# Optimization experiments

Hardware: AMD Instinct MI355X
Metric: run time of the kernel (lower is better)

Reference implementation:

```python
import jax, jax.numpy as jnp
import numpy as np
from jax import lax

IMG_SIZE = 640
STRIDES = (8, 16, 32)
NA = 3          # anchors per level
NC = 80         # classes
CONF_THRESH = 0.001
NMS_THRESH = 0.6
ANCHORS = np.array([[10,13],[16,30],[33,23],[30,61],[62,45],[59,119],[116,90],[156,198],[373,326]], np.float32).reshape(3, 3, 2)

def _make_grids():
    gs, st, aw = [], [], []
    for i, s in enumerate(STRIDES):
        hs = ws = IMG_SIZE // s
        gy, gx = np.meshgrid(np.arange(hs), np.arange(ws), indexing='ij')
        gxy = np.stack([gx, gy], -1).astype(np.float32).reshape(1, hs*ws, 1, 2)
        gs.append(gxy)
        st.append(np.full((1, hs*ws, NA, 2), s, np.float32))
        aw.append(np.tile(ANCHORS[i][None], (hs*ws, 1, 1)))
    return (np.concatenate(gs, 1), np.concatenate(st, 1), np.concatenate(aw, 0)[None])

GRID_CELL, STRIDE_T, ANCH_WH = _make_grids()  # [1,HW,1,2], [1,HW,3,2], [1,HW,3,2]

def _nms_classaware(boxes, score, valid):
    # Greedy NMS, class-aware via coordinate offset already applied to boxes.
    # Faithful to the numpy baseline: w,h = max(1e-28, .), areas without +1.
    x1, y1, x2, y2 = boxes[:, 0], boxes[:, 1], boxes[:, 2], boxes[:, 3]
    areas = (x2 - x1) * (y2 - y1)
    order = jnp.argsort(-score)
    N = boxes.shape[0]
    def body(i, state):
        supp, keep = state
        idx = order[i]
        active = jnp.logical_and(jnp.logical_not(supp[idx]), valid[idx])
        keep = keep.at[idx].set(active)
        xx1 = jnp.maximum(x1[idx], x1)
        yy1 = jnp.maximum(y1[idx], y1)
        xx2 = jnp.minimum(x2[idx], x2)
        yy2 = jnp.minimum(y2[idx], y2)
        w = jnp.maximum(1e-28, xx2 - xx1)
        h = jnp.maximum(1e-28, yy2 - yy1)
        inter = w * h
        iou = inter / (areas[idx] + areas - inter)
        newsupp = jnp.logical_and(iou > NMS_THRESH, active)
        newsupp = newsupp.at[idx].set(False)
        return jnp.logical_or(supp, newsupp), keep
    supp0 = jnp.zeros((N,), bool)
    keep0 = jnp.zeros((N,), bool)
    _, keep = lax.fori_loop(0, N, body, (supp0, keep0))
    return keep

def _decode_and_nms(pred_s, pred_m, pred_l):
    objs, clss, regs = [], [], []
    for pred in (pred_s, pred_m, pred_l):
        B, C, H, W = pred.shape
        p = pred.transpose(0, 2, 3, 1).reshape(B, H*W, C)
        objs.append(p[..., :NA].reshape(B, H*W*NA, 1))
        clss.append(p[..., NA:NA*(1+NC)].reshape(B, H*W*NA, NC))
        regs.append(p[..., NA*(1+NC):].reshape(B, H*W, NA, 4))
    obj_pred = jnp.concatenate(objs, axis=1)   # [B, N, 1]
    cls_pred = jnp.concatenate(clss, axis=1)   # [B, N, NC]
    reg_pred = jnp.concatenate(regs, axis=1)   # [B, HW, 3, 4]
    grid = jnp.asarray(GRID_CELL)
    stride = jnp.asarray(STRIDE_T)
    anch = jnp.asarray(ANCH_WH)
    B = reg_pred.shape[0]
    c_xy = (jax.nn.sigmoid(reg_pred[..., :2]) + grid) * stride
    b_wh = jnp.exp(reg_pred[..., 2:]) * anch
    xywh = jnp.concatenate([c_xy, b_wh], -1).reshape(B, -1, 4)
    x1y1 = xywh[..., :2] - xywh[..., 2:] / 2
    x2y2 = xywh[..., :2] + xywh[..., 2:] / 2
    boxes = jnp.clip(jnp.concatenate([x1y1, x2y2], -1) / IMG_SIZE, 0.0, 1.0)[0]  # [N,4]
    obj_s = jax.nn.sigmoid(obj_pred)[0]                     # [N,1]
    scores_all = jax.nn.softmax(cls_pred[0], axis=1) * obj_s  # [N,NC]
    cls_ind = jnp.argmax(scores_all, axis=1)                # [N]
    score = jnp.max(scores_all, axis=1)                     # [N]
    valid = score >= CONF_THRESH
    # class-aware NMS: offset normalized boxes by 2*class so classes never overlap
    boxes_off = boxes + cls_ind[:, None].astype(boxes.dtype) * 2.0
    keep = _nms_classaware(lax.stop_gradient(boxes_off), lax.stop_gradient(score), valid)
    out = jnp.concatenate([
        boxes,                                    # 4 cols
        score[:, None],                           # 1 col
        cls_ind[:, None].astype(boxes.dtype),     # 1 col (non-diff)
        keep[:, None].astype(boxes.dtype),        # 1 col (non-diff)
    ], axis=1)                                    # [N, 7]
    return out

def setup_inputs() -> dict:
    key = jax.random.key(0)
    k1, k2, k3 = jax.random.split(key, 3)
    return {
        'pred_s': jax.random.normal(k1, (1, 255, 80, 80), jnp.float32),
        'pred_m': jax.random.normal(k2, (1, 255, 40, 40), jnp.float32),
        'pred_l': jax.random.normal(k3, (1, 255, 20, 20), jnp.float32),
    }

def reference(pred_s, pred_m, pred_l):
    return _decode_and_nms(pred_s, pred_m, pred_l)
```

## Files before the change

kernel.cpp:

```cpp
#include <hip/hip_runtime.h>
#include <cstdint>

#define NPRED 25200
#define NPOS  8400
#define NCLS  80
#define CAP   512
#define CSTRIDE 16
#define MW    8
#define NCHUNK 132

__device__ __forceinline__ float sigmoidf_(float x) { return 1.0f / (1.0f + expf(-x)); }

__global__ __launch_bounds__(64) void decode_kernel(
    const float* __restrict__ ps, const float* __restrict__ pm, const float* __restrict__ pl,
    float* __restrict__ out, int* __restrict__ counts,
    float4* __restrict__ g_boxin, uint64_t* __restrict__ g_key)
{
    int chunk = blockIdx.x;
    int a     = blockIdx.y;
    int t     = threadIdx.x;

    const float* p; int HW, W, base, si; float stride; int w0;
    if (chunk < 100)      { p = ps; HW = 6400; W = 80; stride = 8.f;  base = 0;    si = 0; w0 = chunk * 64; }
    else if (chunk < 125) { p = pm; HW = 1600; W = 40; stride = 16.f; base = 6400; si = 1; w0 = (chunk - 100) * 64; }
    else                  { p = pl; HW = 400;  W = 20; stride = 32.f; base = 8000; si = 2; w0 = (chunk - 125) * 64; }

    int local = w0 + t;
    bool valid = local < HW;
    int lclamp = valid ? local : (HW - 1);

    __shared__ float lds[NCLS * 64];

    const float* cbase = p + (size_t)(3 + a * NCLS) * HW;
    int lane_c = t >> 4;
    int j      = (t & 15) << 2;
    int off    = w0 + j; if (off > HW - 4) off = HW - 4;

    float4 vreg[20];
#pragma unroll
    for (int r0 = 0; r0 < 20; r0++)
        vreg[r0] = *(const float4*)(cbase + (size_t)(r0 * 4 + lane_c) * HW + off);
    float objl = p[(size_t)a * HW + lclamp];
    const float* rb = p + (size_t)(3 + 3 * NCLS + a * 4) * HW + lclamp;
    float tx = rb[0], ty = rb[(size_t)HW], tw = rb[(size_t)2 * HW], th = rb[(size_t)3 * HW];
#pragma unroll
    for (int r0 = 0; r0 < 20; r0++)
        *(float4*)&lds[(r0 * 4 + lane_c) * 64 + j] = vreg[r0];
    __syncthreads();

    float m = -INFINITY;
#pragma unroll 16
    for (int c = 0; c < NCLS; c++) m = fmaxf(m, lds[c * 64 + t]);
    float s = 0.f;
#pragma unroll 16
    for (int c = 0; c < NCLS; c++) {
        float e = expf(lds[c * 64 + t] - m);
        lds[c * 64 + t] = e;
        s += e;
    }
    float obj = sigmoidf_(objl);
    float best = -1.f; int bi = 0;
#pragma unroll 16
    for (int c = 0; c < NCLS; c++) {
        float sc = lds[c * 64 + t] / s * obj;
        if (sc > best) { best = sc; bi = c; }
    }

    if (!valid) return;

    const float AW[9] = {10.f,16.f,33.f, 30.f,62.f,59.f, 116.f,156.f,373.f};
    const float AH[9] = {13.f,30.f,23.f, 61.f,45.f,119.f, 90.f,198.f,326.f};
    float aw = AW[si*3 + a], ah = AH[si*3 + a];

    int y = local / W;
    int x = local - y * W;
    float cx = (sigmoidf_(tx) + (float)x) * stride;
    float cy = (sigmoidf_(ty) + (float)y) * stride;
    float bw = expf(tw) * aw;
    float bh = expf(th) * ah;
    float x1 = fminf(fmaxf((cx - bw / 2.f) / 640.f, 0.f), 1.f);
    float y1 = fminf(fmaxf((cy - bh / 2.f) / 640.f, 0.f), 1.f);
    float x2 = fminf(fmaxf((cx + bw / 2.f) / 640.f, 0.f), 1.f);
    float y2 = fminf(fmaxf((cy + bh / 2.f) / 640.f, 0.f), 1.f);

    int g = (base + local) * 3 + a;
    float clsf = (float)bi;
    float* o = out + (size_t)g * 7;
    o[0] = x1; o[1] = y1; o[2] = x2; o[3] = y2;
    o[4] = best; o[5] = clsf; o[6] = 0.f;

    if (best >= 0.001f) {
        int slot = atomicAdd(&counts[bi * CSTRIDE], 1);
        if (slot < CAP) {
            float off2 = clsf * 2.0f;
            g_boxin[bi * CAP + slot] = make_float4(x1 + off2, y1 + off2,
                                                   x2 + off2, y2 + off2);
            unsigned u = __float_as_uint(best);
            u = (u & 0x80000000u) ? ~u : (u | 0x80000000u);
            g_key[bi * CAP + slot] = ((uint64_t)(~u) << 15) | (uint64_t)g;
        }
    }
}

__global__ __launch_bounds__(256) void nms_sort_kernel(
    const int* __restrict__ counts, const uint64_t* __restrict__ g_key,
    const float4* __restrict__ g_boxin, float4* __restrict__ g_sbox,
    int* __restrict__ g_sg)
{
    int c  = blockIdx.x;
    int i0 = blockIdx.y << 6;
    int n = counts[c * CSTRIDE]; if (n > CAP) n = CAP;
    if (i0 >= n) return;
    int tid = threadIdx.x;

    __shared__ uint64_t key[CAP];
    for (int i = tid; i < n; i += 256) key[i] = g_key[c * CAP + i];
    __syncthreads();

    int item = i0 + (tid >> 2);
    int sub  = tid & 3;
    bool act = item < n;
    int r = 0;
    uint64_t k = 0;
    if (act) {
        k = key[item];
        int nq = (n + 3) >> 2;
        int lo = sub * nq; if (lo > n) lo = n;
        int hi = lo + nq;  if (hi > n) hi = n;
        int jj = lo;
        for (; jj + 8 <= hi; jj += 8) {
            int t0 = key[jj]   < k, t1 = key[jj+1] < k;
            int t2 = key[jj+2] < k, t3 = key[jj+3] < k;
            int t4 = key[jj+4] < k, t5 = key[jj+5] < k;
            int t6 = key[jj+6] < k, t7 = key[jj+7] < k;
            r += t0 + t1 + t2 + t3 + t4 + t5 + t6 + t7;
        }
        for (; jj < hi; jj++) r += (key[jj] < k);
    }
    r += __shfl_xor(r, 1);
    r += __shfl_xor(r, 2);
    if (act && sub == 0) {
        g_sbox[c * CAP + r] = g_boxin[c * CAP + item];
        g_sg[c * CAP + r] = (int)(k & 0x7FFF);
    }
}

__global__ __launch_bounds__(256) void nms_build_kernel(
    const int* __restrict__ counts, const float4* __restrict__ g_sbox,
    uint64_t* __restrict__ g_mask)
{
    int c = blockIdx.x;
    int w = blockIdx.y;
    int n = counts[c * CSTRIDE]; if (n > CAP) n = CAP;
    int j0 = w << 6;
    if (j0 >= n) return;
    int j1 = j0 + 64; if (j1 > n) j1 = n;
    int cnt = j1 - j0;
    int tid = threadIdx.x;

    __shared__ float4 sb[64];
    if (tid < 64) {
        float4 sv = make_float4(3e30f, 3e30f, 3e30f, 3e30f);
        if (tid < cnt) sv = g_sbox[c * CAP + j0 + tid];
        sb[tid] = sv;
    }
    __syncthreads();

    uint64_t* gm = g_mask + (size_t)c * MW * CAP + (size_t)w * CAP;
    for (int i = tid; i < n; i += 256) {
        float4 b4 = g_sbox[c * CAP + i];
        float Ai = (b4.z - b4.x) * (b4.w - b4.y);
        uint64_t bits = 0;
        if (i + 1 < j1) {
#pragma unroll 8
            for (int jq = 0; jq < 64; jq++) {
                float4 bj = sb[jq];
                float xx1 = fmaxf(b4.x, bj.x);
                float yy1 = fmaxf(b4.y, bj.y);
                float xx2 = fminf(b4.z, bj.z);
                float yy2 = fminf(b4.w, bj.w);
                float ww = fmaxf(1e-28f, xx2 - xx1);
                float hh = fmaxf(1e-28f, yy2 - yy1);
                float inter = ww * hh;
                float Aj = (bj.z - bj.x) * (bj.w - bj.y);
                float iou = inter / ((Ai + Aj) - inter);
                if ((j0 + jq) > i && iou > 0.6f) bits |= 1ull << jq;
            }
        }
        gm[i] = bits;
    }
}

__global__ __launch_bounds__(64) void nms_scan_kernel(
    const int* __restrict__ counts, const int* __restrict__ g_sg,
    const uint64_t* __restrict__ g_mask, float* __restrict__ out)
{
    int c = blockIdx.x;
    int n = counts[c * CSTRIDE]; if (n > CAP) n = CAP;
    int nw = (n + 63) >> 6;
    int lane = threadIdx.x;

    const uint64_t* gm = g_mask + (size_t)c * MW * CAP;
    const int* sg = g_sg + c * CAP;

    uint64_t removed = 0;
    for (int w = 0; w < nw; w++) {
        uint64_t rw = __shfl(removed, w);
        int row = (w << 6) + lane;
        uint64_t diag = (row < n) ? gm[w * CAP + row] : 0ull;
        int rem = n - (w << 6);
        uint64_t valid = (rem >= 64) ? ~0ull : ((1ull << rem) - 1ull);
        uint64_t nulls = __ballot(diag == 0ull);
        uint64_t cand = ~rw & valid;
        uint64_t kw = 0;
        uint64_t it = cand & ~nulls;
        while (it) {
            int b = __ffsll((unsigned long long)it) - 1;
            kw |= 1ull << b;
            uint64_t db = __shfl(diag, b);
            it &= ~db; cand &= ~db;
            it &= ~(1ull << b);
        }
        kw |= cand & nulls;

        int g  = lane >> 3;
        int wp = lane & 7;
        uint64_t acc = 0;
        if (wp < nw) {
            uint64_t mybits = kw & (0xFFull << (g * 8));
            while (mybits) {
                int b = __ffsll((unsigned long long)mybits) - 1;
                mybits &= mybits - 1;
                acc |= gm[wp * CAP + ((w << 6) + b)];
            }
        }
        acc |= __shfl_xor(acc, 8);
        acc |= __shfl_xor(acc, 16);
        acc |= __shfl_xor(acc, 32);
        if (lane < MW) removed |= acc;

        if (row < n && ((kw >> lane) & 1))
            out[(size_t)sg[row] * 7 + 6] = 1.0f;
    }
}

extern "C" void kernel_launch(void* const* d_in, const int* in_sizes, int n_in,
                              void* d_out, int out_size, void* d_ws, size_t ws_size,
                              hipStream_t stream) {
    const float* ps = (const float*)d_in[0];
    const float* pm = (const float*)d_in[1];
    const float* pl = (const float*)d_in[2];
    float* out = (float*)d_out;

    char* ws = (char*)d_ws;
    int*      counts  = (int*)ws;
    float4*   g_boxin = (float4*)(ws + 8192);
    uint64_t* g_key   = (uint64_t*)(ws + 663552);
    float4*   g_sbox  = (float4*)(ws + 991232);
    int*      g_sg    = (int*)(ws + 1646592);
    uint64_t* g_mask  = (uint64_t*)(ws + 1810432);

    hipMemsetAsync(counts, 0, 8192, stream);
    decode_kernel<<<dim3(NCHUNK, 3), 64, 0, stream>>>(ps, pm, pl, out, counts, g_boxin, g_key);
    nms_sort_kernel<<<dim3(NCLS, MW), 256, 0, stream>>>(counts, g_key, g_boxin, g_sbox, g_sg);
    nms_build_kernel<<<dim3(NCLS, MW), 256, 0, stream>>>(counts, g_sbox, g_mask);
    nms_scan_kernel<<<NCLS, 64, 0, stream>>>(counts, g_sg, g_mask, out);
}
```

Measured before the change: 111.4 us.

## Fuse NMS sort, mask build and scan into one per-class kernel

Replaces the three NMS kernels (sort, mask build, scan) with a single kernel that runs one 256-thread block per class. Sorted boxes, indices and the IoU mask now live in shared memory instead of global workspace. This removes two kernel launches and the global round trips between stages. In exchange each class gets one block of 256 threads instead of up to eight blocks per stage, so less of the GPU works in parallel, and the block's shared-memory footprint grows to roughly 46 KB.

```diff
diff --git a/kernel.cpp b/kernel.cpp
--- a/kernel.cpp
+++ b/kernel.cpp
@@ -102,145 +102,113 @@
     }
 }
 
-__global__ __launch_bounds__(256) void nms_sort_kernel(
-    const int* __restrict__ counts, const uint64_t* __restrict__ g_key,
-    const float4* __restrict__ g_boxin, float4* __restrict__ g_sbox,
-    int* __restrict__ g_sg)
+__global__ __launch_bounds__(256) void nms_fused_kernel(
+    const int* __restrict__ counts, const float4* __restrict__ g_boxin,
+    const uint64_t* __restrict__ g_key, float* __restrict__ out)
 {
-    int c  = blockIdx.x;
-    int i0 = blockIdx.y << 6;
+    int c = blockIdx.x;
     int n = counts[c * CSTRIDE]; if (n > CAP) n = CAP;
-    if (i0 >= n) return;
+    if (n == 0) return;
+    int nw = (n + 63) >> 6;
     int tid = threadIdx.x;
 
     __shared__ uint64_t key[CAP];
+    __shared__ float4   sbox[CAP];
+    __shared__ int      sg[CAP];
+    __shared__ uint64_t mask[MW * CAP];
+    __shared__ uint64_t keptw[MW];
+
     for (int i = tid; i < n; i += 256) key[i] = g_key[c * CAP + i];
-    __syncthreads();
-
-    int item = i0 + (tid >> 2);
-    int sub  = tid & 3;
-    bool act = item < n;
-    int r = 0;
-    uint64_t k = 0;
-    if (act) {
-        k = key[item];
-        int nq = (n + 3) >> 2;
-        int lo = sub * nq; if (lo > n) lo = n;
-        int hi = lo + nq;  if (hi > n) hi = n;
-        int jj = lo;
-        for (; jj + 8 <= hi; jj += 8) {
+    for (int i = n + tid; i < nw * 64; i += 256)
+        sbox[i] = make_float4(3e30f, 3e30f, 3e30f, 3e30f);
+    __syncthreads();
+
+    for (int i = tid; i < n; i += 256) {
+        uint64_t k = key[i];
+        int r = 0, jj = 0;
+        for (; jj + 8 <= n; jj += 8) {
             int t0 = key[jj]   < k, t1 = key[jj+1] < k;
             int t2 = key[jj+2] < k, t3 = key[jj+3] < k;
             int t4 = key[jj+4] < k, t5 = key[jj+5] < k;
             int t6 = key[jj+6] < k, t7 = key[jj+7] < k;
             r += t0 + t1 + t2 + t3 + t4 + t5 + t6 + t7;
         }
-        for (; jj < hi; jj++) r += (key[jj] < k);
-    }
-    r += __shfl_xor(r, 1);
-    r += __shfl_xor(r, 2);
-    if (act && sub == 0) {
-        g_sbox[c * CAP + r] = g_boxin[c * CAP + item];
-        g_sg[c * CAP + r] = (int)(k & 0x7FFF);
-    }
-}
-
-__global__ __launch_bounds__(256) void nms_build_kernel(
-    const int* __restrict__ counts, const float4* __restrict__ g_sbox,
-    uint64_t* __restrict__ g_mask)
-{
-    int c = blockIdx.x;
-    int w = blockIdx.y;
-    int n = counts[c * CSTRIDE]; if (n > CAP) n = CAP;
-    int j0 = w << 6;
-    if (j0 >= n) return;
-    int j1 = j0 + 64; if (j1 > n) j1 = n;
-    int cnt = j1 - j0;
-    int tid = threadIdx.x;
-
-    __shared__ float4 sb[64];
+        for (; jj < n; jj++) r += (key[jj] < k);
+        sbox[r] = g_boxin[c * CAP + i];
+        sg[r] = (int)(k & 0x7FFF);
+    }
+    __syncthreads();
+
+    for (int w = 0; w < nw; w++) {
+        int j0 = w << 6;
+        int j1 = j0 + 64; if (j1 > n) j1 = n;
+        for (int i = tid; i < n; i += 256) {
+            float4 b4 = sbox[i];
+            float Ai = (b4.z - b4.x) * (b4.w - b4.y);
+            uint64_t bits = 0;
+            if (i + 1 < j1) {
+#pragma unroll 8
+                for (int jq = 0; jq < 64; jq++) {
+                    float4 bj = sbox[j0 + jq];
+                    float xx1 = fmaxf(b4.x, bj.x);
+                    float yy1 = fmaxf(b4.y, bj.y);
+                    float xx2 = fminf(b4.z, bj.z);
+                    float yy2 = fminf(b4.w, bj.w);
+                    float ww = fmaxf(1e-28f, xx2 - xx1);
+                    float hh = fmaxf(1e-28f, yy2 - yy1);
+                    float inter = ww * hh;
+                    float Aj = (bj.z - bj.x) * (bj.w - bj.y);
+                    float iou = inter / ((Ai + Aj) - inter);
+                    if ((j0 + jq) > i && (j0 + jq) < j1 && iou > 0.6f)
+                        bits |= 1ull << jq;
+                }
+            }
+            mask[w * CAP + i] = bits;
+        }
+    }
+    __syncthreads();
+
     if (tid < 64) {
-        float4 sv = make_float4(3e30f, 3e30f, 3e30f, 3e30f);
-        if (tid < cnt) sv = g_sbox[c * CAP + j0 + tid];
-        sb[tid] = sv;
-    }
-    __syncthreads();
-
-    uint64_t* gm = g_mask + (size_t)c * MW * CAP + (size_t)w * CAP;
-    for (int i = tid; i < n; i += 256) {
-        float4 b4 = g_sbox[c * CAP + i];
-        float Ai = (b4.z - b4.x) * (b4.w - b4.y);
-        uint64_t bits = 0;
-        if (i + 1 < j1) {
-#pragma unroll 8
-            for (int jq = 0; jq < 64; jq++) {
-                float4 bj = sb[jq];
-                float xx1 = fmaxf(b4.x, bj.x);
-                float yy1 = fmaxf(b4.y, bj.y);
-                float xx2 = fminf(b4.z, bj.z);
-                float yy2 = fminf(b4.w, bj.w);
-                float ww = fmaxf(1e-28f, xx2 - xx1);
-                float hh = fmaxf(1e-28f, yy2 - yy1);
-                float inter = ww * hh;
-                float Aj = (bj.z - bj.x) * (bj.w - bj.y);
-                float iou = inter / ((Ai + Aj) - inter);
-                if ((j0 + jq) > i && iou > 0.6f) bits |= 1ull << jq;
+        int lane = tid;
+        uint64_t removed = 0;
+        for (int w = 0; w < nw; w++) {
+            uint64_t rw = __shfl(removed, w);
+            int row = (w << 6) + lane;
+            uint64_t diag = (row < n) ? mask[w * CAP + row] : 0ull;
+            int rem = n - (w << 6);
+            uint64_t valid = (rem >= 64) ? ~0ull : ((1ull << rem) - 1ull);
+            uint64_t nulls = __ballot(diag == 0ull);
+            uint64_t cand = ~rw & valid;
+            uint64_t kw = 0;
+            uint64_t it = cand & ~nulls;
+            while (it) {
+                int b = __ffsll((unsigned long long)it) - 1;
+                kw |= 1ull << b;
+                uint64_t db = __shfl(diag, b);
+                it &= ~db; cand &= ~db;
+                it &= ~(1ull << b);
             }
-        }
-        gm[i] = bits;
-    }
-}
-
-__global__ __launch_bounds__(64) void nms_scan_kernel(
-    const int* __restrict__ counts, const int* __restrict__ g_sg,
-    const uint64_t* __restrict__ g_mask, float* __restrict__ out)
-{
-    int c = blockIdx.x;
-    int n = counts[c * CSTRIDE]; if (n > CAP) n = CAP;
-    int nw = (n + 63) >> 6;
-    int lane = threadIdx.x;
-
-    const uint64_t* gm = g_mask + (size_t)c * MW * CAP;
-    const int* sg = g_sg + c * CAP;
-
-    uint64_t removed = 0;
-    for (int w = 0; w < nw; w++) {
-        uint64_t rw = __shfl(removed, w);
-        int row = (w << 6) + lane;
-        uint64_t diag = (row < n) ? gm[w * CAP + row] : 0ull;
-        int rem = n - (w << 6);
-        uint64_t valid = (rem >= 64) ? ~0ull : ((1ull << rem) - 1ull);
-        uint64_t nulls = __ballot(diag == 0ull);
-        uint64_t cand = ~rw & valid;
-        uint64_t kw = 0;
-        uint64_t it = cand & ~nulls;
-        while (it) {
-            int b = __ffsll((unsigned long long)it) - 1;
-            kw |= 1ull << b;
-            uint64_t db = __shfl(diag, b);
-            it &= ~db; cand &= ~db;
-            it &= ~(1ull << b);
-        }
-        kw |= cand & nulls;
-
-        int g  = lane >> 3;
-        int wp = lane & 7;
-        uint64_t acc = 0;
-        if (wp < nw) {
-            uint64_t mybits = kw & (0xFFull << (g * 8));
-            while (mybits) {
-                int b = __ffsll((unsigned long long)mybits) - 1;
-                mybits &= mybits - 1;
-                acc |= gm[wp * CAP + ((w << 6) + b)];
+            kw |= cand & nulls;
+
+            int g  = lane >> 3;
+            int wp = lane & 7;
+            uint64_t acc = 0;
+            if (wp < nw) {
+                uint64_t mybits = kw & (0xFFull << (g * 8));
+                while (mybits) {
+                    int b = __ffsll((unsigned long long)mybits) - 1;
+                    mybits &= mybits - 1;
+                    acc |= mask[wp * CAP + ((w << 6) + b)];
+                }
             }
-        }
-        acc |= __shfl_xor(acc, 8);
-        acc |= __shfl_xor(acc, 16);
-        acc |= __shfl_xor(acc, 32);
-        if (lane < MW) removed |= acc;
-
-        if (row < n && ((kw >> lane) & 1))
-            out[(size_t)sg[row] * 7 + 6] = 1.0f;
+            acc |= __shfl_xor(acc, 8);
+            acc |= __shfl_xor(acc, 16);
+            acc |= __shfl_xor(acc, 32);
+            if (lane < MW) removed |= acc;
+
+            if (row < n && ((kw >> lane) & 1))
+                out[(size_t)sg[row] * 7 + 6] = 1.0f;
+        }
     }
 }
 
@@ -256,13 +224,8 @@
     int*      counts  = (int*)ws;
     float4*   g_boxin = (float4*)(ws + 8192);
     uint64_t* g_key   = (uint64_t*)(ws + 663552);
-    float4*   g_sbox  = (float4*)(ws + 991232);
-    int*      g_sg    = (int*)(ws + 1646592);
-    uint64_t* g_mask  = (uint64_t*)(ws + 1810432);
 
     hipMemsetAsync(counts, 0, 8192, stream);
     decode_kernel<<<dim3(NCHUNK, 3), 64, 0, stream>>>(ps, pm, pl, out, counts, g_boxin, g_key);
-    nms_sort_kernel<<<dim3(NCLS, MW), 256, 0, stream>>>(counts, g_key, g_boxin, g_sbox, g_sg);
-    nms_build_kernel<<<dim3(NCLS, MW), 256, 0, stream>>>(counts, g_sbox, g_mask);
-    nms_scan_kernel<<<NCLS, 64, 0, stream>>>(counts, g_sg, g_mask, out);
+    nms_fused_kernel<<<NCLS, 256, 0, stream>>>(counts, g_boxin, g_key, out);
 }
```

After: 164.5 us. 1.48x slower.
